# Kernel optimization log

Hardware: AMD Instinct MI355X
Metric: run time of the kernel (lower is better)

Reference implementation:

```python
import jax, jax.numpy as jnp
import numpy as np

D1, D2, K = 2, 4, 2   # dilation1, dilation2, kernel_size
EPS = 1e-5            # BatchNorm eps (torch default)


def _dilated_nodes(queue, dilation, new_node):
    # queue: (L, bs, C, 1); take every `dilation`-th entry, append new node,
    # lay out as (bs, C, k) then flatten to (bs, C*k) matching torch's
    # cat(..., axis=2).reshape(bs, -1).
    nodes = jnp.concatenate([queue[0::dilation], new_node[None]], axis=0)  # (k, bs, C, 1)
    bs = new_node.shape[0]
    return jnp.moveaxis(nodes[..., 0], 0, -1).reshape(bs, -1)  # (bs, C*k)


def _bn_eval(h, scale, bias, mean, var):
    return (h - mean) * (scale * jax.lax.rsqrt(var + EPS)) + bias


def setup_inputs() -> dict:
    key = jax.random.key(0)
    ks = jax.random.split(key, 17)
    bs, din, mid, out = 16384, 512, 1024, 512
    in_ch = din * K          # 1024
    return {
        "x": jax.random.normal(ks[0], (bs, din, 1), jnp.float32),
        "conv1_queue": jax.random.normal(ks[1], (D1 * (K - 1), bs, din, 1), jnp.float32),
        "conv2_queue": jax.random.normal(ks[2], (D2 * (K - 1), bs, mid, 1), jnp.float32),
        "w1": jax.random.normal(ks[3], (mid, in_ch), jnp.float32) / np.sqrt(in_ch),
        "b1": jax.random.normal(ks[4], (mid,), jnp.float32) * 0.01,
        "w2": jax.random.normal(ks[5], (out, mid * K), jnp.float32) / np.sqrt(mid * K),
        "b2": jax.random.normal(ks[6], (out,), jnp.float32) * 0.01,
        "w_skip": jax.random.normal(ks[7], (out, in_ch), jnp.float32) / np.sqrt(in_ch),
        "b_skip": jax.random.normal(ks[8], (out,), jnp.float32) * 0.01,
        "bn1_scale": jax.random.uniform(ks[9], (mid,), jnp.float32, 0.5, 1.5),
        "bn1_bias": jax.random.normal(ks[10], (mid,), jnp.float32) * 0.01,
        "bn1_mean": jax.random.normal(ks[11], (mid,), jnp.float32) * 0.1,
        "bn1_var": jax.random.uniform(ks[12], (mid,), jnp.float32, 0.5, 1.5),
        "bn2_scale": jax.random.uniform(ks[13], (out,), jnp.float32, 0.5, 1.5),
        "bn2_bias": jax.random.normal(ks[14], (out,), jnp.float32) * 0.01,
        "bn2_mean": jax.random.normal(ks[15], (out,), jnp.float32) * 0.1,
        "bn2_var": jax.random.uniform(ks[16], (out,), jnp.float32, 0.5, 1.5),
    }


def reference(x, conv1_queue, conv2_queue, w1, b1, w2, b2, w_skip, b_skip,
              bn1_scale, bn1_bias, bn1_mean, bn1_var,
              bn2_scale, bn2_bias, bn2_mean, bn2_var):
    # l1_input: (bs, in_ch) = (bs, din*K)
    l1_input = _dilated_nodes(conv1_queue, D1, x)
    conv1_out = l1_input @ w1.T + b1                       # (bs, mid)
    conv1_out = _bn_eval(jax.nn.relu(conv1_out), bn1_scale, bn1_bias, bn1_mean, bn1_var)

    # l2_input: (bs, mid*K)
    l2_input = _dilated_nodes(conv2_queue, D2, conv1_out[:, :, None])
    conv2_out = l2_input @ w2.T + b2                       # (bs, out)
    conv2_out = conv2_out + (l1_input @ w_skip.T + b_skip)  # skip (in_ch != out_ch)
    conv2_out = jax.nn.relu(conv2_out)
    conv2_out = _bn_eval(conv2_out, bn2_scale, bn2_bias, bn2_mean, bn2_var)
    return conv2_out[:, :, None]                           # (bs, out, 1)
```

## Files before the change

kernel.cpp:

```cpp
#include <hip/hip_runtime.h>
#include <hip/hip_bf16.h>


#define BS   16384
#define DIN  512
#define MID  1024
#define NOUT 512
#define KA2  3072
#define BN_EPS 1e-5f

typedef __attribute__((ext_vector_type(8))) short bf16x8;
typedef __attribute__((ext_vector_type(4))) float floatx4;

#define GLDS(g, l) __builtin_amdgcn_global_load_lds( \
    (const __attribute__((address_space(1))) void*)(g), \
    (__attribute__((address_space(3))) void*)(l), 16, 0, 0)

__device__ __forceinline__ void cvt_store8(const float* __restrict__ src,
                                           __hip_bfloat16* __restrict__ dst) {
    float4 u = *(const float4*)src;
    float4 v = *(const float4*)(src + 4);
    __hip_bfloat16 tmp[8] __attribute__((aligned(16)));
    tmp[0] = __float2bfloat16(u.x); tmp[1] = __float2bfloat16(u.y);
    tmp[2] = __float2bfloat16(u.z); tmp[3] = __float2bfloat16(u.w);
    tmp[4] = __float2bfloat16(v.x); tmp[5] = __float2bfloat16(v.y);
    tmp[6] = __float2bfloat16(v.z); tmp[7] = __float2bfloat16(v.w);
    *(float4*)dst = *(const float4*)tmp;
}

__device__ __forceinline__ void cvt_store8_s2(const float* __restrict__ src,
                                              __hip_bfloat16* __restrict__ dst) {
    __hip_bfloat16 tmp[8] __attribute__((aligned(16)));
#pragma unroll
    for (int i = 0; i < 8; ++i) tmp[i] = __float2bfloat16(src[2 * i]);
    *(float4*)dst = *(const float4*)tmp;
}

#define T_Q2  ((long)BS * 128)
#define T_Q1X ((long)BS * 64)
#define T_W1  (1024L * 1024 / 8)
#define T_W2  (512L * 3072 / 8)
#define T_ALL (T_Q2 + T_Q1X + T_W1 + T_W2)

__global__ __launch_bounds__(256) void prep_all_kernel(
    const float* __restrict__ x, const float* __restrict__ q1,
    const float* __restrict__ q2, const float* __restrict__ w1,
    const float* __restrict__ w2, const float* __restrict__ wsk,
    __hip_bfloat16* __restrict__ A2,
    __hip_bfloat16* __restrict__ w1p, __hip_bfloat16* __restrict__ w2p)
{
    long id = (long)blockIdx.x * 256 + threadIdx.x;
    if (id < T_Q2) {
        long b = id >> 7;
        int j = (int)(id & 127) << 3;
        cvt_store8(q2 + b * MID + j, A2 + b * KA2 + j);
    } else if (id < T_Q2 + T_Q1X) {
        long id2 = id - T_Q2;
        long b = id2 >> 6;
        int j = (int)(id2 & 63) << 3;
        cvt_store8(q1 + b * DIN + j, A2 + b * KA2 + 2048 + j);
        cvt_store8(x  + b * DIN + j, A2 + b * KA2 + 2560 + j);
    } else if (id < T_Q2 + T_Q1X + T_W1) {
        long t = id - (T_Q2 + T_Q1X);
        long o8 = t * 8;
        int m = (int)(o8 >> 10), k0 = (int)(o8 & 1023);
        const float* src = w1 + m * 1024 + ((k0 < 512) ? 2 * k0 : 2 * (k0 - 512) + 1);
        cvt_store8_s2(src, w1p + o8);
    } else {
        long t = id - (T_Q2 + T_Q1X + T_W1);
        long o8 = t * 8;
        int o = (int)(o8 / 3072), k0 = (int)(o8 - (long)o * 3072);
        const float* src;
        if (k0 < 1024)      src = w2 + o * 2048 + 2 * k0;
        else if (k0 < 2048) src = w2 + o * 2048 + 2 * (k0 - 1024) + 1;
        else if (k0 < 2560) src = wsk + o * 1024 + 2 * (k0 - 2048);
        else                src = wsk + o * 1024 + 2 * (k0 - 2560) + 1;
        cvt_store8_s2(src, w2p + o8);
    }
}


#define PBAR() do { __builtin_amdgcn_sched_barrier(0); \
                    __builtin_amdgcn_s_barrier(); \
                    __builtin_amdgcn_sched_barrier(0); } while (0)
#define LGKM0() asm volatile("s_waitcnt lgkmcnt(0)" ::: "memory")
#define VMW(n)  asm volatile("s_waitcnt vmcnt(" #n ")" ::: "memory")

#define STAGE_TILE(G, STRIDE, ROWBLK, K0, LBASE) do { \
    _Pragma("unroll") for (int c_ = 0; c_ < 4; ++c_) { \
        int f0_ = (c_ * 8 + wave) * 64; \
        int f_  = f0_ + lane; \
        int sr_ = f_ >> 3, cc_ = f_ & 7; \
        GLDS((G) + (size_t)((ROWBLK) + sr_) * (STRIDE) + (K0) + ((cc_ ^ (sr_ & 7)) << 3), \
             ((short*)(LBASE)) + f0_ * 8); \
    } } while (0)

#define READ_A(BUF, IH) do { \
    _Pragma("unroll") for (int i_ = 0; i_ < 4; ++i_) { \
        int r_ = wm * 128 + (IH) * 64 + i_ * 16 + (lane & 15); \
        _Pragma("unroll") for (int kk_ = 0; kk_ < 2; ++kk_) { \
            int cc_ = (kk_ * 4 + (lane >> 4)) ^ (r_ & 7); \
            a[i_][kk_] = *(const bf16x8*)&As[BUF][r_][cc_ * 8]; \
        } } } while (0)

#define READ_B(BUF, JH) do { \
    _Pragma("unroll") for (int j_ = 0; j_ < 2; ++j_) { \
        int r_ = wn * 64 + (JH) * 32 + j_ * 16 + (lane & 15); \
        _Pragma("unroll") for (int kk_ = 0; kk_ < 2; ++kk_) { \
            int cc_ = (kk_ * 4 + (lane >> 4)) ^ (r_ & 7); \
            b[(JH) * 2 + j_][kk_] = *(const bf16x8*)&Bs[BUF][r_][cc_ * 8]; \
        } } } while (0)

#define MFMA_Q(IH, JH) do { \
    __builtin_amdgcn_s_setprio(1); \
    _Pragma("unroll") for (int i_ = 0; i_ < 4; ++i_) \
    _Pragma("unroll") for (int j_ = 0; j_ < 2; ++j_) \
    _Pragma("unroll") for (int kk_ = 0; kk_ < 2; ++kk_) \
        acc[(IH) * 4 + i_][(JH) * 2 + j_] = __builtin_amdgcn_mfma_f32_16x16x32_bf16( \
            a[i_][kk_], b[(JH) * 2 + j_][kk_], acc[(IH) * 4 + i_][(JH) * 2 + j_], 0, 0, 0); \
    __builtin_amdgcn_s_setprio(0); \
} while (0)

__global__ __launch_bounds__(512, 2) void gemm1_8ph(
    const __hip_bfloat16* __restrict__ Ag,
    const __hip_bfloat16* __restrict__ Bg,
    const float* __restrict__ bias,
    const float* __restrict__ bn_s, const float* __restrict__ bn_b,
    const float* __restrict__ bn_m, const float* __restrict__ bn_v,
    __hip_bfloat16* __restrict__ hout)
{
    __shared__ __align__(16) short As[2][256][64];
    __shared__ __align__(16) short Bs[2][256][64];

    const int t = threadIdx.x;
    const int lane = t & 63;
    const int wave = t >> 6;
    const int wm = wave >> 2;
    const int wn = wave & 3;

    const int p = blockIdx.x;
    const int m0 = ((p & 7) + 8 * ((p >> 3) & 7)) * 256;
    const int n0 = (p >> 6) * 256;

    floatx4 acc[8][4];
#pragma unroll
    for (int i = 0; i < 8; ++i)
#pragma unroll
        for (int j = 0; j < 4; ++j)
            acc[i][j] = (floatx4){0.f, 0.f, 0.f, 0.f};

    bf16x8 a[4][2], b[4][2];

    STAGE_TILE(Bg, 1024, n0, 0,  Bs[0]);
    STAGE_TILE(Ag, KA2,  m0, 0,  As[0]);
    STAGE_TILE(Bg, 1024, n0, 64, Bs[1]);
    STAGE_TILE(Ag, KA2,  m0, 64, As[1]);
    VMW(0);
    __builtin_amdgcn_s_barrier();

    for (int it = 0; it < 8; ++it) {
        const bool more = (it < 7);
        const int kn = it * 128 + 128;

        READ_A(0, 0); READ_B(0, 0);
        PBAR(); LGKM0(); MFMA_Q(0, 0); PBAR();
        READ_B(0, 1);
        PBAR(); LGKM0(); MFMA_Q(0, 1); PBAR();
        READ_A(0, 1);
        if (more) STAGE_TILE(Bg, 1024, n0, kn, Bs[0]);
        PBAR(); LGKM0(); MFMA_Q(1, 1); PBAR();
        if (more) { VMW(4); } else { VMW(0); }
        if (more) STAGE_TILE(Ag, KA2, m0, kn, As[0]);
        PBAR(); MFMA_Q(1, 0); PBAR();

        READ_A(1, 0); READ_B(1, 0);
        PBAR(); LGKM0(); MFMA_Q(0, 0); PBAR();
        READ_B(1, 1);
        PBAR(); LGKM0(); MFMA_Q(0, 1); PBAR();
        READ_A(1, 1);
        if (more) STAGE_TILE(Bg, 1024, n0, kn + 64, Bs[1]);
        PBAR(); LGKM0(); MFMA_Q(1, 1); PBAR();
        VMW(4);
        if (more) STAGE_TILE(Ag, KA2, m0, kn + 64, As[1]);
        PBAR(); MFMA_Q(1, 0); PBAR();
    }

#pragma unroll
    for (int j = 0; j < 4; ++j) {
        int col = n0 + wn * 64 + j * 16 + (lane & 15);
        float bias_v = bias[col];
        float scale = bn_s[col] * rsqrtf(bn_v[col] + BN_EPS);
        float mean = bn_m[col], beta = bn_b[col];
#pragma unroll
        for (int i = 0; i < 8; ++i) {
            int rbase = m0 + wm * 128 + i * 16 + (lane >> 4) * 4;
#pragma unroll
            for (int r = 0; r < 4; ++r) {
                float v = acc[i][j][r] + bias_v;
                v = fmaxf(v, 0.f);
                v = (v - mean) * scale + beta;
                hout[(size_t)(rbase + r) * KA2 + col] = __float2bfloat16(v);
            }
        }
    }
}

template <int EPI>
__global__ __launch_bounds__(256) void mfma_gemm(
    const __hip_bfloat16* __restrict__ A, const __hip_bfloat16* __restrict__ B,
    int K, long strideA,
    const float* __restrict__ bias_a, const float* __restrict__ bias_b,
    const float* __restrict__ bn_s, const float* __restrict__ bn_b,
    const float* __restrict__ bn_m, const float* __restrict__ bn_v,
    __hip_bfloat16* __restrict__ hout, float* __restrict__ fout, int strideOut)
{
    __shared__ short Asl[128 * 32];
    __shared__ short Bsl[128 * 32];

    const int t = threadIdx.x;
    const int lane = t & 63;
    const int wave = t >> 6;
    const int wm = wave >> 1, wn = wave & 1;

    const int p = blockIdx.x;
    const int m0 = ((p & 7) + 8 * ((p >> 3) & 15)) * 128;
    const int n0 = ((p >> 3) >> 4) * 128;

    floatx4 acc[4][4];
#pragma unroll
    for (int i = 0; i < 4; ++i)
#pragma unroll
        for (int j = 0; j < 4; ++j)
            acc[i][j] = (floatx4){0.f, 0.f, 0.f, 0.f};

    for (int k0 = 0; k0 < K; k0 += 32) {
#pragma unroll
        for (int c = 0; c < 2; ++c) {
            int fb = c * 256 + wave * 64;
            int f = fb + lane;
            GLDS(A + (size_t)(m0 + (f >> 2)) * strideA + k0 + (f & 3) * 8,
                 Asl + fb * 8);
            GLDS(B + (size_t)(n0 + (f >> 2)) * (size_t)K + k0 + (f & 3) * 8,
                 Bsl + fb * 8);
        }
        __syncthreads();

        bf16x8 af[4], bfr[4];
#pragma unroll
        for (int i = 0; i < 4; ++i)
            af[i] = *(const bf16x8*)&Asl[(wm * 64 + i * 16 + (lane & 15)) * 32 +
                                         (lane >> 4) * 8];
#pragma unroll
        for (int j = 0; j < 4; ++j)
            bfr[j] = *(const bf16x8*)&Bsl[(wn * 64 + j * 16 + (lane & 15)) * 32 +
                                          (lane >> 4) * 8];
#pragma unroll
        for (int i = 0; i < 4; ++i)
#pragma unroll
            for (int j = 0; j < 4; ++j)
                acc[i][j] = __builtin_amdgcn_mfma_f32_16x16x32_bf16(
                    af[i], bfr[j], acc[i][j], 0, 0, 0);
        __syncthreads();
    }

#pragma unroll
    for (int j = 0; j < 4; ++j) {
        int col = n0 + wn * 64 + j * 16 + (lane & 15);
        float bias = bias_a[col];
        if (EPI == 2) bias += bias_b[col];
        float scale = bn_s[col] * rsqrtf(bn_v[col] + BN_EPS);
        float mean = bn_m[col], beta = bn_b[col];
#pragma unroll
        for (int i = 0; i < 4; ++i) {
            int rbase = m0 + wm * 64 + i * 16 + (lane >> 4) * 4;
#pragma unroll
            for (int r = 0; r < 4; ++r) {
                float v = acc[i][j][r] + bias;
                v = fmaxf(v, 0.f);
                v = (v - mean) * scale + beta;
                if (EPI == 1)
                    hout[(size_t)(rbase + r) * strideOut + col] = __float2bfloat16(v);
                else
                    fout[(size_t)(rbase + r) * strideOut + col] = v;
            }
        }
    }
}

extern "C" void kernel_launch(void* const* d_in, const int* in_sizes, int n_in,
                              void* d_out, int out_size, void* d_ws, size_t ws_size,
                              hipStream_t stream) {
    const float* x   = (const float*)d_in[0];
    const float* q1  = (const float*)d_in[1];
    const float* q2  = (const float*)d_in[2];
    const float* w1  = (const float*)d_in[3];
    const float* b1  = (const float*)d_in[4];
    const float* w2  = (const float*)d_in[5];
    const float* b2  = (const float*)d_in[6];
    const float* wsk = (const float*)d_in[7];
    const float* bsk = (const float*)d_in[8];
    const float* s1  = (const float*)d_in[9];
    const float* bb1 = (const float*)d_in[10];
    const float* m1  = (const float*)d_in[11];
    const float* v1  = (const float*)d_in[12];
    const float* s2  = (const float*)d_in[13];
    const float* bb2 = (const float*)d_in[14];
    const float* m2  = (const float*)d_in[15];
    const float* v2  = (const float*)d_in[16];
    float* out = (float*)d_out;

    size_t needA2 = (size_t)BS * KA2 * sizeof(__hip_bfloat16);
    size_t needW  = ((size_t)1024 * 1024 + (size_t)512 * 3072) * sizeof(__hip_bfloat16);
    char* base;
    if (ws_size >= needA2 + needW)
        base = (char*)d_ws;
    else
        base = (char*)d_in[2] + (size_t)BS * MID * sizeof(float);
    __hip_bfloat16* A2  = (__hip_bfloat16*)base;
    __hip_bfloat16* w1p = (__hip_bfloat16*)(base + needA2);
    __hip_bfloat16* w2p = w1p + 1024 * 1024;

    prep_all_kernel<<<dim3((int)(T_ALL / 256)), dim3(256), 0, stream>>>(
        x, q1, q2, w1, w2, wsk, A2, w1p, w2p);

    gemm1_8ph<<<dim3(256), dim3(512), 0, stream>>>(
        A2 + 2048, w1p, b1, s1, bb1, m1, v1, A2 + 1024);

    mfma_gemm<2><<<dim3(512), dim3(256), 0, stream>>>(
        A2, w2p, 3072, KA2,
        b2, bsk, s2, bb2, m2, v2,
        nullptr, out, NOUT);
}
```

Measured before the change: 539.4 us.

## Replace second GEMM with double-buffered 256x128 tile pipelined kernel

Replaces the simple single-buffered 128x128 MFMA GEMM for the second layer with a 512-thread kernel using 256x128 tiles and K=64 stages. LDS is double-buffered and XOR-swizzled, global-to-LDS loads are interleaved with MFMA phases, and s_setprio is raised around the MFMA blocks. The aim is to hide global load latency and cut barrier stalls and LDS bank conflicts in the K=3072 GEMM. The larger tile raises register and LDS use, and the grid drops to 256 blocks, which can lower occupancy.

```diff
diff --git a/kernel.cpp b/kernel.cpp
--- a/kernel.cpp
+++ b/kernel.cpp
@@ -86,6 +86,7 @@
 #define LGKM0() asm volatile("s_waitcnt lgkmcnt(0)" ::: "memory")
 #define VMW(n)  asm volatile("s_waitcnt vmcnt(" #n ")" ::: "memory")
 
+
 #define STAGE_TILE(G, STRIDE, ROWBLK, K0, LBASE) do { \
     _Pragma("unroll") for (int c_ = 0; c_ < 4; ++c_) { \
         int f0_ = (c_ * 8 + wave) * 64; \
@@ -205,83 +206,122 @@
     }
 }
 
-template <int EPI>
-__global__ __launch_bounds__(256) void mfma_gemm(
-    const __hip_bfloat16* __restrict__ A, const __hip_bfloat16* __restrict__ B,
-    int K, long strideA,
+
+#define STAGE_A2T(K0, LBASE) do { \
+    _Pragma("unroll") for (int c_ = 0; c_ < 4; ++c_) { \
+        int f0_ = (c_ * 8 + wave) * 64; \
+        int f_  = f0_ + lane; \
+        int sr_ = f_ >> 3, cc_ = f_ & 7; \
+        GLDS(Ag + (size_t)(m0 + sr_) * KA2 + (K0) + ((cc_ ^ (sr_ & 7)) << 3), \
+             ((short*)(LBASE)) + f0_ * 8); \
+    } } while (0)
+
+#define STAGE_B2T(K0, LBASE) do { \
+    _Pragma("unroll") for (int c_ = 0; c_ < 2; ++c_) { \
+        int f0_ = (c_ * 8 + wave) * 64; \
+        int f_  = f0_ + lane; \
+        int sr_ = f_ >> 3, cc_ = f_ & 7; \
+        GLDS(Bg + (size_t)(n0 + sr_) * KA2 + (K0) + ((cc_ ^ (sr_ & 7)) << 3), \
+             ((short*)(LBASE)) + f0_ * 8); \
+    } } while (0)
+
+#define READ_A2G(BUF, IH) do { \
+    _Pragma("unroll") for (int i_ = 0; i_ < 4; ++i_) { \
+        int r_ = wm * 128 + (IH) * 64 + i_ * 16 + (lane & 15); \
+        _Pragma("unroll") for (int kk_ = 0; kk_ < 2; ++kk_) { \
+            int cc_ = (kk_ * 4 + (lane >> 4)) ^ (r_ & 7); \
+            a[i_][kk_] = *(const bf16x8*)&As2[BUF][r_][cc_ * 8]; \
+        } } } while (0)
+
+#define READ_B2G(BUF) do { \
+    _Pragma("unroll") for (int j_ = 0; j_ < 2; ++j_) { \
+        int r_ = wn * 32 + j_ * 16 + (lane & 15); \
+        _Pragma("unroll") for (int kk_ = 0; kk_ < 2; ++kk_) { \
+            int cc_ = (kk_ * 4 + (lane >> 4)) ^ (r_ & 7); \
+            br[j_][kk_] = *(const bf16x8*)&Bs2[BUF][r_][cc_ * 8]; \
+        } } } while (0)
+
+#define MFMA_H(IH) do { \
+    __builtin_amdgcn_s_setprio(1); \
+    _Pragma("unroll") for (int i_ = 0; i_ < 4; ++i_) \
+    _Pragma("unroll") for (int j_ = 0; j_ < 2; ++j_) \
+    _Pragma("unroll") for (int kk_ = 0; kk_ < 2; ++kk_) \
+        acc[(IH) * 4 + i_][j_] = __builtin_amdgcn_mfma_f32_16x16x32_bf16( \
+            a[i_][kk_], br[j_][kk_], acc[(IH) * 4 + i_][j_], 0, 0, 0); \
+    __builtin_amdgcn_s_setprio(0); \
+} while (0)
+
+__global__ __launch_bounds__(512, 2) void gemm2_8ph(
+    const __hip_bfloat16* __restrict__ Ag,
+    const __hip_bfloat16* __restrict__ Bg,
     const float* __restrict__ bias_a, const float* __restrict__ bias_b,
     const float* __restrict__ bn_s, const float* __restrict__ bn_b,
     const float* __restrict__ bn_m, const float* __restrict__ bn_v,
-    __hip_bfloat16* __restrict__ hout, float* __restrict__ fout, int strideOut)
+    float* __restrict__ fout)
 {
-    __shared__ short Asl[128 * 32];
-    __shared__ short Bsl[128 * 32];
+    __shared__ __align__(16) short As2[2][256][64];
+    __shared__ __align__(16) short Bs2[2][128][64];
 
     const int t = threadIdx.x;
     const int lane = t & 63;
     const int wave = t >> 6;
-    const int wm = wave >> 1, wn = wave & 1;
+    const int wm = wave >> 2;
+    const int wn = wave & 3;
 
     const int p = blockIdx.x;
-    const int m0 = ((p & 7) + 8 * ((p >> 3) & 15)) * 128;
-    const int n0 = ((p >> 3) >> 4) * 128;
-
-    floatx4 acc[4][4];
-#pragma unroll
-    for (int i = 0; i < 4; ++i)
-#pragma unroll
-        for (int j = 0; j < 4; ++j)
+    const int m0 = ((p & 7) + 8 * ((p >> 3) & 7)) * 256;
+    const int n0 = (p >> 6) * 128;
+
+    floatx4 acc[8][2];
+#pragma unroll
+    for (int i = 0; i < 8; ++i)
+#pragma unroll
+        for (int j = 0; j < 2; ++j)
             acc[i][j] = (floatx4){0.f, 0.f, 0.f, 0.f};
 
-    for (int k0 = 0; k0 < K; k0 += 32) {
-#pragma unroll
-        for (int c = 0; c < 2; ++c) {
-            int fb = c * 256 + wave * 64;
-            int f = fb + lane;
-            GLDS(A + (size_t)(m0 + (f >> 2)) * strideA + k0 + (f & 3) * 8,
-                 Asl + fb * 8);
-            GLDS(B + (size_t)(n0 + (f >> 2)) * (size_t)K + k0 + (f & 3) * 8,
-                 Bsl + fb * 8);
-        }
-        __syncthreads();
-
-        bf16x8 af[4], bfr[4];
-#pragma unroll
-        for (int i = 0; i < 4; ++i)
-            af[i] = *(const bf16x8*)&Asl[(wm * 64 + i * 16 + (lane & 15)) * 32 +
-                                         (lane >> 4) * 8];
-#pragma unroll
-        for (int j = 0; j < 4; ++j)
-            bfr[j] = *(const bf16x8*)&Bsl[(wn * 64 + j * 16 + (lane & 15)) * 32 +
-                                          (lane >> 4) * 8];
-#pragma unroll
-        for (int i = 0; i < 4; ++i)
-#pragma unroll
-            for (int j = 0; j < 4; ++j)
-                acc[i][j] = __builtin_amdgcn_mfma_f32_16x16x32_bf16(
-                    af[i], bfr[j], acc[i][j], 0, 0, 0);
-        __syncthreads();
-    }
-
-#pragma unroll
-    for (int j = 0; j < 4; ++j) {
-        int col = n0 + wn * 64 + j * 16 + (lane & 15);
-        float bias = bias_a[col];
-        if (EPI == 2) bias += bias_b[col];
+    bf16x8 a[4][2], br[2][2];
+
+    STAGE_B2T(0,  Bs2[0]);
+    STAGE_A2T(0,  As2[0]);
+    STAGE_B2T(64, Bs2[1]);
+    VMW(0);
+    __builtin_amdgcn_s_barrier();
+
+    for (int it = 0; it < 24; ++it) {
+        const bool more = (it < 23);
+        const int kn = it * 128;
+
+        VMW(2);
+        READ_A2G(0, 0); READ_B2G(0);
+        STAGE_A2T(kn + 64, As2[1]);
+        PBAR(); LGKM0(); MFMA_H(0); PBAR();
+        READ_A2G(0, 1);
+        if (more) STAGE_B2T(kn + 128, Bs2[0]);
+        PBAR(); LGKM0(); MFMA_H(1); PBAR();
+        if (more) { VMW(2); } else { VMW(0); }
+        READ_A2G(1, 0); READ_B2G(1);
+        if (more) STAGE_A2T(kn + 128, As2[0]);
+        PBAR(); LGKM0(); MFMA_H(0); PBAR();
+        READ_A2G(1, 1);
+        if (more) STAGE_B2T(kn + 192, Bs2[1]);
+        PBAR(); LGKM0(); MFMA_H(1); PBAR();
+    }
+
+#pragma unroll
+    for (int j = 0; j < 2; ++j) {
+        int col = n0 + wn * 32 + j * 16 + (lane & 15);
+        float bias_v = bias_a[col] + bias_b[col];
         float scale = bn_s[col] * rsqrtf(bn_v[col] + BN_EPS);
         float mean = bn_m[col], beta = bn_b[col];
 #pragma unroll
-        for (int i = 0; i < 4; ++i) {
-            int rbase = m0 + wm * 64 + i * 16 + (lane >> 4) * 4;
+        for (int i = 0; i < 8; ++i) {
+            int rbase = m0 + wm * 128 + i * 16 + (lane >> 4) * 4;
 #pragma unroll
             for (int r = 0; r < 4; ++r) {
-                float v = acc[i][j][r] + bias;
+                float v = acc[i][j][r] + bias_v;
                 v = fmaxf(v, 0.f);
                 v = (v - mean) * scale + beta;
-                if (EPI == 1)
-                    hout[(size_t)(rbase + r) * strideOut + col] = __float2bfloat16(v);
-                else
-                    fout[(size_t)(rbase + r) * strideOut + col] = v;
+                fout[(size_t)(rbase + r) * NOUT + col] = v;
             }
         }
     }
@@ -326,8 +366,6 @@
     gemm1_8ph<<<dim3(256), dim3(512), 0, stream>>>(
         A2 + 2048, w1p, b1, s1, bb1, m1, v1, A2 + 1024);
 
-    mfma_gemm<2><<<dim3(512), dim3(256), 0, stream>>>(
-        A2, w2p, 3072, KA2,
-        b2, bsk, s2, bb2, m2, v2,
-        nullptr, out, NOUT);
-}
+    gemm2_8ph<<<dim3(256), dim3(512), 0, stream>>>(
+        A2, w2p, b2, bsk, s2, bb2, m2, v2, out);
+}
```

Result: faster. 516.7 us (-4.2%).
